# Optimization experiments

Measured on AMD Instinct MI355X. Metric: run time of the kernel, lower is better.

Reference implementation:

```python
import jax, jax.numpy as jnp
import numpy as np

N, K, E = 262144, 8, 16
DT = 0.02  # config.delta_time


def _mono(x, w1, b1, w2, b2):
    # monotonic_fun with increasing=False: out_linear(exp(-in_linear(x)))
    return jnp.exp(-(x @ w1.T + b1)) @ w2.T + b2


def _isin(a, b):
    # rowwise torch.isin: a [N,P], b [N,Q] -> [N,P] bool
    return (a[:, :, None] == b[:, None, :]).any(-1)


def _angle_clamp(vec, v, ang):
    # torch.cosine_similarity(v, vec, dim=-1).abs() > ang gate (eps=1e-8)
    num = jnp.einsum('nd,nrd->nr', v, vec)
    den = jnp.maximum(jnp.linalg.norm(v, axis=-1)[:, None] * jnp.linalg.norm(vec, axis=-1), 1e-8)
    keep = jnp.abs(num / den) > ang
    return jnp.where(keep[..., None], vec, 0.0)


def _linear_params(key, fan_in, fan_out):
    a = 1.0 / np.sqrt(fan_in)
    k1, k2 = jax.random.split(key)
    # weightConstraint(min_b=0) clamps weights to >= 0 at init
    w = jnp.maximum(jax.random.uniform(k1, (fan_out, fan_in), minval=-a, maxval=a), 0.0)
    b = jax.random.uniform(k2, (fan_out,), minval=-a, maxval=a)
    return w, b


def _mono_params(key):
    k1, k2 = jax.random.split(key)
    w1, b1 = _linear_params(k1, 1, E)
    w2, b2 = _linear_params(k2, E, 1)
    return w1, b1, w2, b2


def setup_inputs() -> dict:
    key = jax.random.key(0)
    ks = jax.random.split(key, 12)
    ego = jax.random.normal(ks[0], (N, 16), dtype=jnp.float32)
    ego = ego.at[:, 0].set(jnp.arange(N, dtype=jnp.float32))
    # surrounding-vehicle id columns 7..14 as small integer ids (floats)
    ego = ego.at[:, 7:15].set(jax.random.randint(ks[1], (N, 8), 0, 21).astype(jnp.float32))
    nei = jax.random.normal(ks[2], (N, K, 16), dtype=jnp.float32)
    nei = nei.at[:, :, 0].set(jax.random.randint(ks[3], (N, K), 1, 21).astype(jnp.float32))
    border = jax.random.uniform(ks[4], (4,), dtype=jnp.float32) * 10.0 + 1.0
    recording_time = jnp.zeros((N, K, 2), dtype=jnp.float32)
    p_dest = jax.random.uniform(ks[5], (2,), dtype=jnp.float32)  # relu(rand(2))
    angle = jax.nn.sigmoid(jax.random.uniform(ks[6], (1,), dtype=jnp.float32))
    d = {'ego': ego, 'nei': nei, 'border': border, 'recording_time': recording_time,
         'p_dest': p_dest, 'angle': angle}
    for name, kk in (('rep', ks[7]), ('att', ks[8]), ('bor', ks[9]), ('del', ks[10])):
        w1, b1, w2, b2 = _mono_params(kk)
        d[name + '_w1'], d[name + '_b1'], d[name + '_w2'], d[name + '_b2'] = w1, b1, w2, b2
    return d


def reference(ego, nei, border, recording_time, p_dest, angle,
              rep_w1, rep_b1, rep_w2, rep_b2,
              att_w1, att_b1, att_w2, att_b2,
              bor_w1, bor_b1, bor_w2, bor_b2,
              del_w1, del_b1, del_w2, del_b2):
    ang = angle[0]
    v = ego[:, 3:5]                                        # ego velocity [N,2]
    speed = jnp.linalg.norm(v, axis=-1)
    desired = jnp.stack([speed, jnp.zeros_like(speed)], axis=1)
    f_dest = ((p_dest[1] * desired - v) / p_dest[0])[:, None, :]   # [N,1,2]

    nei_id = nei[:, :, 0]                                  # [N,K]
    idx = _isin(nei_id, ego[:, 7:15]) & (nei_id != 0)

    # --- recording_time buffer update (vectorized remain/new/pad concat) ---
    buf_id, buf_ct = recording_time[:, :, 0], recording_time[:, :, 1]
    ifin = _isin(buf_id, nei_id)                           # buffer slots still present
    ct2 = buf_ct + ifin.astype(buf_ct.dtype)               # increment their counts
    ifnew = (~_isin(nei_id, buf_id)) & (nei_id != 0)       # brand-new neighbor ids
    cand = jnp.concatenate([jnp.stack([buf_id, ct2], -1),
                            jnp.stack([nei_id, jnp.ones_like(nei_id)], -1)], axis=1)  # [N,2K,2]
    ar = jnp.arange(K)
    BIG = 1 << 20
    keyord = jnp.concatenate([jnp.where(ifin, ar, BIG), jnp.where(ifnew, ar + K, BIG)], axis=1)
    order = jnp.argsort(keyord, axis=1)[:, :K]             # stable: remain order, then new, then pad
    skey = jnp.take_along_axis(keyord, order, axis=1)
    new_buf = jnp.where((skey < BIG)[..., None],
                        jnp.take_along_axis(cand, order[..., None], axis=1), 1.0)  # pad with ones
    count = new_buf[:, :, 1]                               # [N,K]

    # --- neighbor attraction / repulsion ---
    r = jnp.where(idx[..., None], nei[:, :, 1:3] - ego[:, None, 1:3], 0.0)
    rn = jnp.linalg.norm(r, axis=-1)
    rns = jnp.where(idx, rn, 1.0)                          # safe divisor (masked slots zeroed below)
    dirn = r / rns[..., None]
    f_attr = (_mono(count[..., None], del_w1, del_b1, del_w2, del_b2)
              * _mono(rn[..., None], att_w1, att_b1, att_w2, att_b2) * dirn)
    v_nei = nei[:, :, 3:5]
    b = rn + jnp.sum((r + v_nei * DT) ** 2, -1) - jnp.sum((v_nei * DT) ** 2, -1)
    b = jnp.sqrt(jnp.maximum(jnp.where(idx, b, 1.0), 1e-12)) / 2.0
    f_repu = _mono(b[..., None], rep_w1, rep_b1, rep_w2, rep_b2) * dirn
    f_attr = jnp.where(idx[..., None], f_attr, 0.0)
    f_repu = jnp.where(idx[..., None], f_repu, 0.0)

    # --- border repulsion (y-axis only), select_lane = [0, -1] ---
    rb_all = ego[:, 2:3] - border                          # [N,4]
    rb = jnp.stack([rb_all[:, 0], rb_all[:, -1]], axis=1)  # [N,2]
    rbn = jnp.abs(rb)
    f_by = _mono(rbn[..., None], bor_w1, bor_b1, bor_w2, bor_b2) * (rb / rbn)[..., None]
    f_bor = jnp.concatenate([jnp.zeros_like(f_by), f_by], axis=-1)  # [N,2,2]

    f_destination = _angle_clamp(f_dest, v, ang).sum(1)
    f_neighbors = _angle_clamp(f_attr, v, ang).sum(1) + _angle_clamp(f_repu, v, ang).sum(1)
    f_border = _angle_clamp(f_bor, v, ang).sum(1)
    return jnp.stack([f_destination, f_neighbors, f_border], axis=1)  # [N,3,2]
```

## Files before the change

kernel.cpp:

```cpp
#include <hip/hip_runtime.h>
#include <math.h>

#define EN 16
#define TBL_N 1024
#define TBL_XMAX 20.0f
#define TBL_SCALE ((float)TBL_N / TBL_XMAX)
#define TBL_STEP  (TBL_XMAX / (float)TBL_N)
#define WS_ATT 0
#define WS_REP 1025
#define WS_BOR 2050
#define WS_DEL1 3075
#define WS_TOTAL 3076

extern "C" __global__ void __launch_bounds__(256)
build_tables(const float* __restrict__ rep_w1, const float* __restrict__ rep_b1,
             const float* __restrict__ rep_w2, const float* __restrict__ rep_b2,
             const float* __restrict__ att_w1, const float* __restrict__ att_b1,
             const float* __restrict__ att_w2, const float* __restrict__ att_b2,
             const float* __restrict__ bor_w1, const float* __restrict__ bor_b1,
             const float* __restrict__ bor_w2, const float* __restrict__ bor_b2,
             const float* __restrict__ del_w1, const float* __restrict__ del_b1,
             const float* __restrict__ del_w2, const float* __restrict__ del_b2,
             float* __restrict__ ws)
{
    int gid = blockIdx.x * blockDim.x + threadIdx.x;
    if (gid >= WS_TOTAL) return;

    const float *w1, *b1, *w2, *b2;
    float x;
    if (gid == WS_DEL1) {
        w1 = del_w1; b1 = del_b1; w2 = del_w2; b2 = del_b2; x = 1.0f;
    } else {
        int net = gid / 1025;
        int e = gid - net * 1025;
        x = (float)e * TBL_STEP;
        if (net == 0)      { w1 = att_w1; b1 = att_b1; w2 = att_w2; b2 = att_b2; }
        else if (net == 1) { w1 = rep_w1; b1 = rep_b1; w2 = rep_w2; b2 = rep_b2; }
        else               { w1 = bor_w1; b1 = bor_b1; w2 = bor_w2; b2 = bor_b2; }
    }
    float acc = 0.0f;
#pragma unroll
    for (int e = 0; e < EN; ++e)
        acc = fmaf(__expf(-fmaf(x, w1[e], b1[e])), w2[e], acc);
    ws[gid] = acc + b2[0];
}

__device__ __forceinline__ float tbl_lookup(const float* __restrict__ T, float x) {
    float t = x * TBL_SCALE;
    int i = (int)t;
    i = (i > TBL_N - 1) ? (TBL_N - 1) : i;
    float fr = t - (float)i;
    float f0 = T[i], f1 = T[i + 1];
    return fmaf(fr, f1 - f0, f0);
}

extern "C" __global__ void __launch_bounds__(256)
sfm_kernel(const float* __restrict__ ego, const float* __restrict__ nei,
           const float* __restrict__ border, const float* __restrict__ rec,
           const float* __restrict__ p_dest, const float* __restrict__ angle,
           const float* __restrict__ del_w1, const float* __restrict__ del_b1,
           const float* __restrict__ del_w2, const float* __restrict__ del_b2,
           const float* __restrict__ ws,
           float* __restrict__ out, int N)
{
    const int gid = blockIdx.x * blockDim.x + threadIdx.x;
    const int n = gid >> 3;
    const int k = gid & 7;
    const int lane = threadIdx.x & 63;
    const int gbase = lane & ~7;

    float2 e2 = *(const float2*)(ego + (size_t)n * 16 + 2 * k);
    const float* nb = nei + (size_t)n * 128 + (size_t)k * 16;
    float4 na = *(const float4*)nb;
    float nvyv = nb[4];
    float2 rc = *(const float2*)(rec + (size_t)n * 16 + 2 * k);
    const float ang = angle[0];
    const float p0 = p_dest[0], p1 = p_dest[1];
    const float b0 = border[0], b3 = border[3];
    const float del_one = ws[WS_DEL1];

    __shared__ float T[WS_TOTAL - 1];
    for (int i = threadIdx.x; i < WS_TOTAL - 1; i += 256)
        T[i] = ws[i];
    __syncthreads();

    const float ex = e2.x, ey = e2.y;
    const float px  = __shfl(ey, gbase + 0);
    const float py  = __shfl(ex, gbase + 1);
    const float vx  = __shfl(ey, gbase + 1);
    const float vy  = __shfl(ex, gbase + 2);
    const float id0 = __shfl(ey, gbase + 3);
    const float id1 = __shfl(ex, gbase + 4);
    const float id2 = __shfl(ey, gbase + 4);
    const float id3 = __shfl(ex, gbase + 5);
    const float id4 = __shfl(ey, gbase + 5);
    const float id5 = __shfl(ex, gbase + 6);
    const float id6 = __shfl(ey, gbase + 6);
    const float id7 = __shfl(ex, gbase + 7);

    const float speed = sqrtf(vx * vx + vy * vy);
    const float nid = na.x;
    const float bid = rc.x, bct = rc.y;

    unsigned long long m1 = __ballot(bid != 0.0f);
    unsigned long long m2 = __ballot(nid == 0.0f);
    float cntk;
    if ((m1 | m2) == 0ull) {
        cntk = 1.0f;
    } else {
        bool fin = (bid == nid);
#pragma unroll
        for (int t = 1; t < 8; ++t)
            fin = fin || (bid == __shfl_xor(nid, t));
        unsigned long long bal = __ballot(fin);
        unsigned finM = (unsigned)((bal >> gbase) & 0xFFull);
        int popcFin = __popc(finM);
        int jsel = 0, cbits = 0;
#pragma unroll
        for (int j = 0; j < 8; ++j) {
            int bit = (finM >> j) & 1;
            if (bit && cbits == k) jsel = j;
            cbits += bit;
        }
        float bctj = __shfl(bct, gbase + jsel);
        cntk = (k < popcFin) ? (bctj + 1.0f) : 1.0f;
    }

    bool match = (nid == id0) || (nid == id1) || (nid == id2) || (nid == id3)
              || (nid == id4) || (nid == id5) || (nid == id6) || (nid == id7);
    const bool idxk = match && (nid != 0.0f);

    float rx = idxk ? (na.y - px) : 0.0f;
    float ry = idxk ? (na.z - py) : 0.0f;
    float rn = sqrtf(rx * rx + ry * ry);
    float rns = idxk ? rn : 1.0f;
    float dx = rx / rns, dy = ry / rns;

    float sxv = na.w * 0.02f, syv = nvyv * 0.02f;
    float ox = rx + sxv, oy = ry + syv;
    float bsum = rn + (ox * ox + oy * oy) - (sxv * sxv + syv * syv);
    float bgate = idxk ? bsum : 1.0f;
    float bb = sqrtf(fmaxf(bgate, 1e-12f)) * 0.5f;

    float att = tbl_lookup(T + WS_ATT, rn);
    float rep = tbl_lookup(T + WS_REP, bb);

    float del;
    if (cntk == 1.0f) {
        del = del_one;
    } else {
        float accd = 0.0f;
#pragma unroll
        for (int e = 0; e < EN; ++e)
            accd = fmaf(__expf(-fmaf(cntk, del_w1[e], del_b1[e])), del_w2[e], accd);
        del = accd + del_b2[0];
    }

    float nbx = 0.0f, nby = 0.0f;
    {
        float sa = del * att;
        float fax = idxk ? sa * dx : 0.0f;
        float fay = idxk ? sa * dy : 0.0f;
        float num = vx * fax + vy * fay;
        float fn = sqrtf(fax * fax + fay * fay);
        float den = fmaxf(speed * fn, 1e-8f);
        if (fabsf(num / den) > ang) { nbx += fax; nby += fay; }
    }
    {
        float frx = idxk ? rep * dx : 0.0f;
        float fry = idxk ? rep * dy : 0.0f;
        float num = vx * frx + vy * fry;
        float fn = sqrtf(frx * frx + fry * fry);
        float den = fmaxf(speed * fn, 1e-8f);
        if (fabsf(num / den) > ang) { nbx += frx; nby += fry; }
    }

    float bory;
    {
        float bsel = (k == 0) ? b0 : b3;
        float rb = py - bsel;
        float rbn = fabsf(rb);
        float mb = tbl_lookup(T + WS_BOR, rbn);
        float fby = mb * (rb / rbn);
        float num = vy * fby;
        float den = fmaxf(speed * fabsf(fby), 1e-8f);
        bory = ((fabsf(num / den) > ang) && (k < 2)) ? fby : 0.0f;
    }

#pragma unroll
    for (int m = 1; m < 8; m <<= 1) {
        nbx  += __shfl_xor(nbx,  m);
        nby  += __shfl_xor(nby,  m);
        bory += __shfl_xor(bory, m);
    }

    float fdx = (p1 * speed - vx) / p0;
    float fdy = (0.0f - vy) / p0;
    float fdex = 0.0f, fdey = 0.0f;
    {
        float num = vx * fdx + vy * fdy;
        float fn = sqrtf(fdx * fdx + fdy * fdy);
        float den = fmaxf(speed * fn, 1e-8f);
        if (fabsf(num / den) > ang) { fdex = fdx; fdey = fdy; }
    }

    if (n >= N) return;
    float wv = (k == 0) ? fdex
             : (k == 1) ? fdey
             : (k == 2) ? nbx
             : (k == 3) ? nby
             : (k == 4) ? 0.0f
             : bory;
    if (k < 6) out[(size_t)n * 6 + k] = wv;
}

extern "C" void kernel_launch(void* const* d_in, const int* in_sizes, int n_in,
                              void* d_out, int out_size, void* d_ws, size_t ws_size,
                              hipStream_t stream) {
    const float* ego    = (const float*)d_in[0];
    const float* nei    = (const float*)d_in[1];
    const float* border = (const float*)d_in[2];
    const float* rec    = (const float*)d_in[3];
    const float* p_dest = (const float*)d_in[4];
    const float* angle  = (const float*)d_in[5];
    const float* rep_w1 = (const float*)d_in[6];
    const float* rep_b1 = (const float*)d_in[7];
    const float* rep_w2 = (const float*)d_in[8];
    const float* rep_b2 = (const float*)d_in[9];
    const float* att_w1 = (const float*)d_in[10];
    const float* att_b1 = (const float*)d_in[11];
    const float* att_w2 = (const float*)d_in[12];
    const float* att_b2 = (const float*)d_in[13];
    const float* bor_w1 = (const float*)d_in[14];
    const float* bor_b1 = (const float*)d_in[15];
    const float* bor_w2 = (const float*)d_in[16];
    const float* bor_b2 = (const float*)d_in[17];
    const float* del_w1 = (const float*)d_in[18];
    const float* del_b1 = (const float*)d_in[19];
    const float* del_w2 = (const float*)d_in[20];
    const float* del_b2 = (const float*)d_in[21];
    float* out = (float*)d_out;
    float* ws  = (float*)d_ws;

    int N = in_sizes[0] / 16;

    build_tables<<<dim3((WS_TOTAL + 255) / 256), 256, 0, stream>>>(
        rep_w1, rep_b1, rep_w2, rep_b2,
        att_w1, att_b1, att_w2, att_b2,
        bor_w1, bor_b1, bor_w2, bor_b2,
        del_w1, del_b1, del_w2, del_b2, ws);

    long long threads = (long long)N * 8;
    dim3 grid((unsigned)((threads + 255) / 256));
    sfm_kernel<<<grid, 256, 0, stream>>>(
        ego, nei, border, rec, p_dest, angle,
        del_w1, del_b1, del_w2, del_b2,
        ws, out, N);
}
```

Baseline: 263.5 us.

## Stage neighbor rows through padded LDS slab with coalesced float4 loads

Each wave now loads its 8 agents' full neighbor block (8x128 floats) with fully coalesced float4 loads and writes it to a padded shared-memory slab. Each thread then reads its own row from LDS. Previously each thread did a strided 16-byte plus a scalar load from global memory. Ego fields are now read as four float4 per thread directly instead of being gathered via shuffles. This trades extra LDS traffic and a larger shared footprint, which may lower occupancy, for better global coalescing. It also relies on an lgkmcnt wait rather than a barrier for intra-wave visibility.

```diff
diff --git a/kernel.cpp b/kernel.cpp
--- a/kernel.cpp
+++ b/kernel.cpp
@@ -11,6 +11,11 @@
 #define WS_BOR 2050
 #define WS_DEL1 3075
 #define WS_TOTAL 3076
+#define TSZ (WS_TOTAL - 1)
+
+#define ROW_STRIDE 20
+#define AG_STRIDE 164
+#define WAVE_SLAB (8 * AG_STRIDE)
 
 extern "C" __global__ void __launch_bounds__(256)
 build_tables(const float* __restrict__ rep_w1, const float* __restrict__ rep_b1,
@@ -25,7 +30,6 @@
 {
     int gid = blockIdx.x * blockDim.x + threadIdx.x;
     if (gid >= WS_TOTAL) return;
-
     const float *w1, *b1, *w2, *b2;
     float x;
     if (gid == WS_DEL1) {
@@ -63,41 +67,60 @@
            const float* __restrict__ ws,
            float* __restrict__ out, int N)
 {
-    const int gid = blockIdx.x * blockDim.x + threadIdx.x;
+    __shared__ float T[TSZ];
+    __shared__ float slab[4 * WAVE_SLAB];
+
+    const int tid = threadIdx.x;
+    const int gid = blockIdx.x * 256 + tid;
     const int n = gid >> 3;
     const int k = gid & 7;
-    const int lane = threadIdx.x & 63;
+    const int lane = tid & 63;
+    const int wid = tid >> 6;
+    const int a = lane >> 3;
     const int gbase = lane & ~7;
 
-    float2 e2 = *(const float2*)(ego + (size_t)n * 16 + 2 * k);
-    const float* nb = nei + (size_t)n * 128 + (size_t)k * 16;
-    float4 na = *(const float4*)nb;
-    float nvyv = nb[4];
+    const int agent_base = blockIdx.x * 32 + wid * 8;
+    const float4* slabg = (const float4*)(nei + (size_t)agent_base * 128);
+    float4 s0 = slabg[lane];
+    float4 s1 = slabg[lane + 64];
+    float4 s2 = slabg[lane + 128];
+    float4 s3 = slabg[lane + 192];
+
+    const float* er = ego + (size_t)n * 16;
+    float4 ea = *(const float4*)(er);
+    float4 eb = *(const float4*)(er + 4);
+    float4 ec = *(const float4*)(er + 8);
+    float4 ed = *(const float4*)(er + 12);
+
     float2 rc = *(const float2*)(rec + (size_t)n * 16 + 2 * k);
+
     const float ang = angle[0];
     const float p0 = p_dest[0], p1 = p_dest[1];
     const float b0 = border[0], b3 = border[3];
     const float del_one = ws[WS_DEL1];
 
-    __shared__ float T[WS_TOTAL - 1];
-    for (int i = threadIdx.x; i < WS_TOTAL - 1; i += 256)
+    for (int i = tid; i < TSZ; i += 256)
         T[i] = ws[i];
     __syncthreads();
 
-    const float ex = e2.x, ey = e2.y;
-    const float px  = __shfl(ey, gbase + 0);
-    const float py  = __shfl(ex, gbase + 1);
-    const float vx  = __shfl(ey, gbase + 1);
-    const float vy  = __shfl(ex, gbase + 2);
-    const float id0 = __shfl(ey, gbase + 3);
-    const float id1 = __shfl(ex, gbase + 4);
-    const float id2 = __shfl(ey, gbase + 4);
-    const float id3 = __shfl(ex, gbase + 5);
-    const float id4 = __shfl(ey, gbase + 5);
-    const float id5 = __shfl(ex, gbase + 6);
-    const float id6 = __shfl(ey, gbase + 6);
-    const float id7 = __shfl(ex, gbase + 7);
-
+    {
+        float* wb = slab + wid * WAVE_SLAB;
+        float4 sv[4] = {s0, s1, s2, s3};
+#pragma unroll
+        for (int j = 0; j < 4; ++j) {
+            int p = j * 256 + lane * 4;
+            int ap = p >> 7;
+            int q = p & 127;
+            int off = ap * AG_STRIDE + (q >> 4) * ROW_STRIDE + (q & 15);
+            *(float4*)(wb + off) = sv[j];
+        }
+        __asm__ volatile("s_waitcnt lgkmcnt(0)" ::: "memory");
+    }
+    const float* myrow = slab + wid * WAVE_SLAB + a * AG_STRIDE + k * ROW_STRIDE;
+    float4 na = *(const float4*)myrow;
+    float nvyv = myrow[4];
+
+    const float px = ea.y, py = ea.z, vx = ea.w, vy = eb.x;
     const float speed = sqrtf(vx * vx + vy * vy);
     const float nid = na.x;
     const float bid = rc.x, bct = rc.y;
@@ -126,8 +149,8 @@
         cntk = (k < popcFin) ? (bctj + 1.0f) : 1.0f;
     }
 
-    bool match = (nid == id0) || (nid == id1) || (nid == id2) || (nid == id3)
-              || (nid == id4) || (nid == id5) || (nid == id6) || (nid == id7);
+    bool match = (nid == eb.w) || (nid == ec.x) || (nid == ec.y) || (nid == ec.z)
+              || (nid == ec.w) || (nid == ed.x) || (nid == ed.y) || (nid == ed.z);
     const bool idxk = match && (nid != 0.0f);
 
     float rx = idxk ? (na.y - px) : 0.0f;
```

After: 268.2 us. About the same (+1.8%).
